# Kernel tuning notes

Measured on AMD Instinct MI355X. Metric: run time of the kernel, lower is better.

## Reference

```python
import jax, jax.numpy as jnp
import numpy as np

N_NODES = 50000
N_EDGES = 800000
HIDDEN = 128
EDGE_DIM = 16
COORDS_RANGE = 15.0


def setup_inputs() -> dict:
    key = jax.random.key(0)
    ks = jax.random.split(key, 12)
    h = jax.random.normal(ks[0], (N_NODES, HIDDEN), dtype=jnp.float32)
    x = jax.random.normal(ks[1], (N_NODES, 3), dtype=jnp.float32)
    edge_index = jax.random.randint(ks[2], (2, N_EDGES), 0, N_NODES, dtype=jnp.int64)
    edge_attr = jax.random.normal(ks[3], (N_EDGES, EDGE_DIM), dtype=jnp.float32)
    coord_diff = jax.random.normal(ks[4], (N_EDGES, 3), dtype=jnp.float32)
    flags = jnp.ones((N_NODES, 1), dtype=jnp.float32)
    edge_mask = jnp.ones((N_EDGES, 1), dtype=jnp.float32)
    d_in = 2 * HIDDEN + EDGE_DIM
    # MLP params (xavier-ish scaling; last layer gain 0.001 as in source)
    W1 = jax.random.normal(ks[5], (d_in, HIDDEN), dtype=jnp.float32) * (2.0 / (d_in + HIDDEN)) ** 0.5
    b1 = jnp.zeros((HIDDEN,), dtype=jnp.float32)
    W2 = jax.random.normal(ks[6], (HIDDEN, HIDDEN), dtype=jnp.float32) * (1.0 / HIDDEN) ** 0.5
    b2 = jnp.zeros((HIDDEN,), dtype=jnp.float32)
    W3 = jax.random.normal(ks[7], (HIDDEN, 1), dtype=jnp.float32) * 0.001 * (2.0 / (HIDDEN + 1)) ** 0.5
    return {"h": h, "x": x, "edge_index": edge_index, "edge_attr": edge_attr,
            "coord_diff": coord_diff, "flags": flags, "edge_mask": edge_mask,
            "W1": W1, "b1": b1, "W2": W2, "b2": b2, "W3": W3}


def reference(h, x, edge_index, edge_attr, coord_diff, flags, edge_mask, W1, b1, W2, b2, W3):
    row, col = edge_index[0], edge_index[1]
    # gather node features per edge and concat with edge features: [E, 2H+De]
    msg = jnp.concatenate([h[row], h[col], edge_attr], axis=1)
    z = jax.nn.silu(msg @ W1 + b1)
    z = jax.nn.silu(z @ W2 + b2)
    scale = jnp.tanh(z @ W3)                  # [E, 1]
    trans = coord_diff * scale * COORDS_RANGE # [E, 3]
    # NOTE: source computes `tanns = trans * edge_mask` but never uses it;
    # the aggregation uses the UNmasked trans. Faithfully replicated.
    agg = jax.ops.segment_sum(trans, row, num_segments=x.shape[0])  # [N, 3]
    return (x + agg) * flags
```

## Files before the change

kernel.cpp:

```cpp
#include <hip/hip_runtime.h>

typedef short  short8   __attribute__((ext_vector_type(8)));
typedef float  floatx16 __attribute__((ext_vector_type(16)));

#define HID  128
#define LDM  296
#define LDZ  136
#define NK1  18
#define NK2  8

__device__ __forceinline__ float fast_silu(float v) {
    return __fdividef(v, 1.0f + __expf(-v));
}
__device__ __forceinline__ unsigned short f2bf(float f) {
    union { float f; unsigned int u; } v; v.f = f;
    unsigned int r = v.u + 0x7FFFu + ((v.u >> 16) & 1u);
    return (unsigned short)(r >> 16);
}

__global__ void prep_weights(const float* __restrict__ W1, const float* __restrict__ W2,
                             unsigned short* __restrict__ w1t, unsigned short* __restrict__ w2t)
{
    const int tid = blockIdx.x * 256 + threadIdx.x;
    if (tid < 4 * NK1 * 64) {
        const int tn   = tid / (NK1 * 64);
        const int rem  = tid % (NK1 * 64);
        const int ks   = rem / 64;
        const int lane = rem % 64;
        const int n  = 32 * tn + (lane & 31);
        const int kb = 16 * ks + 8 * (lane >> 5);
        unsigned short o[8];
        #pragma unroll
        for (int j = 0; j < 8; ++j) {
            const int k = kb + j;
            o[j] = (k < 272) ? f2bf(W1[(size_t)k * HID + n]) : (unsigned short)0;
        }
        #pragma unroll
        for (int j = 0; j < 8; ++j) w1t[(size_t)tid * 8 + j] = o[j];
    } else if (tid < 4 * NK1 * 64 + 4 * NK2 * 64) {
        const int id   = tid - 4 * NK1 * 64;
        const int tn   = id / (NK2 * 64);
        const int rem  = id % (NK2 * 64);
        const int ks   = rem / 64;
        const int lane = rem % 64;
        const int n  = 32 * tn + (lane & 31);
        const int kb = 16 * ks + 8 * (lane >> 5);
        #pragma unroll
        for (int j = 0; j < 8; ++j)
            w2t[(size_t)id * 8 + j] = f2bf(W2[(size_t)(kb + j) * HID + n]);
    }
}

__global__ void prep_cast(const float* __restrict__ h, const float* __restrict__ ea,
                          unsigned short* __restrict__ hb, unsigned short* __restrict__ eab,
                          int nh, int nea)
{
    const int total4 = (nh + nea) >> 2;
    for (int i = blockIdx.x * blockDim.x + threadIdx.x; i < total4; i += gridDim.x * blockDim.x) {
        float4 v;
        unsigned short* dst;
        if (i < (nh >> 2)) { v = ((const float4*)h)[i];            dst = hb  + (size_t)i * 4; }
        else               { v = ((const float4*)ea)[i - (nh>>2)]; dst = eab + (size_t)(i - (nh>>2)) * 4; }
        const unsigned int lo = (unsigned int)f2bf(v.x) | ((unsigned int)f2bf(v.y) << 16);
        const unsigned int hi = (unsigned int)f2bf(v.z) | ((unsigned int)f2bf(v.w) << 16);
        *(uint2*)dst = make_uint2(lo, hi);
    }
}

__global__ __launch_bounds__(256, 2) void egnn_mfma_kernel(
    const unsigned short* __restrict__ hb,
    const int* __restrict__ eidx,
    const unsigned short* __restrict__ eab,
    const float* __restrict__ coord_diff,
    const unsigned short* __restrict__ w1t,
    const unsigned short* __restrict__ w2t,
    const float* __restrict__ b1,
    const float* __restrict__ b2,
    const float* __restrict__ W3,
    float* __restrict__ agg,
    int E, int niter)
{
    __shared__ unsigned short s_msg[64][LDM];
    __shared__ unsigned short s_z1[64][LDZ];
    __shared__ float s_z3[64];
    __shared__ int   s_row[64];

    const int t    = threadIdx.x;
    const int lane = t & 63;
    const int w    = t >> 6;
    const int c31  = lane & 31;
    const int hi   = lane >> 5;

    float b1f[16], b2f[16], w3f[16];
    #pragma unroll
    for (int r = 0; r < 16; ++r) {
        const int n = 32 * w + (r & 3) + 8 * (r >> 2) + 4 * hi;
        b1f[r] = b1[n]; b2f[r] = b2[n]; w3f[r] = W3[n];
    }

    for (int it = blockIdx.x; it < niter; it += gridDim.x) {
        const int ebase = it * 64;

        {
            const int e = t >> 2, s = t & 3;
            const int g  = ebase + e;
            const int gc = (g < E) ? g : (E - 1);
            const int row = eidx[gc];
            const int col = eidx[(size_t)E + gc];
            if (s == 0) s_row[e] = row;
            if (t < 64) s_z3[t] = 0.0f;
            const uint4* hr = (const uint4*)(hb + (size_t)row * HID);
            const uint4* hc = (const uint4*)(hb + (size_t)col * HID);
            #pragma unroll
            for (int i = 0; i < 4; ++i) {
                const int q = s + 4 * i;
                *(uint4*)&s_msg[e][q * 8]       = hr[q];
                *(uint4*)&s_msg[e][HID + q * 8] = hc[q];
            }
            const uint4* ea4 = (const uint4*)(eab + (size_t)gc * 16);
            if (s < 2) *(uint4*)&s_msg[e][256 + s * 8] = ea4[s];
            else       *(uint4*)&s_msg[e][256 + s * 8] = make_uint4(0u, 0u, 0u, 0u);
        }
        __syncthreads();

        floatx16 acc0 = {}, acc1 = {};
        #pragma unroll
        for (int ks = 0; ks < NK1; ++ks) {
            const short8 wf = *(const short8*)(w1t + ((size_t)(w * NK1 + ks) * 64 + lane) * 8);
            const short8 a0 = *(const short8*)&s_msg[c31][16 * ks + 8 * hi];
            const short8 a1 = *(const short8*)&s_msg[32 + c31][16 * ks + 8 * hi];
            acc0 = __builtin_amdgcn_mfma_f32_32x32x16_bf16(wf, a0, acc0, 0, 0, 0);
            acc1 = __builtin_amdgcn_mfma_f32_32x32x16_bf16(wf, a1, acc1, 0, 0, 0);
        }
        #pragma unroll
        for (int te = 0; te < 2; ++te) {
            const floatx16& A = te ? acc1 : acc0;
            const int e = 32 * te + c31;
            #pragma unroll
            for (int q = 0; q < 4; ++q) {
                const float f0 = fast_silu(A[4*q+0] + b1f[4*q+0]);
                const float f1 = fast_silu(A[4*q+1] + b1f[4*q+1]);
                const float f2 = fast_silu(A[4*q+2] + b1f[4*q+2]);
                const float f3 = fast_silu(A[4*q+3] + b1f[4*q+3]);
                const unsigned int lo = (unsigned int)f2bf(f0) | ((unsigned int)f2bf(f1) << 16);
                const unsigned int hw = (unsigned int)f2bf(f2) | ((unsigned int)f2bf(f3) << 16);
                *(uint2*)&s_z1[e][32 * w + 8 * q + 4 * hi] = make_uint2(lo, hw);
            }
        }
        __syncthreads();

        floatx16 g0 = {}, g1 = {};
        #pragma unroll
        for (int ks = 0; ks < NK2; ++ks) {
            const short8 wf = *(const short8*)(w2t + ((size_t)(w * NK2 + ks) * 64 + lane) * 8);
            const short8 a0 = *(const short8*)&s_z1[c31][16 * ks + 8 * hi];
            const short8 a1 = *(const short8*)&s_z1[32 + c31][16 * ks + 8 * hi];
            g0 = __builtin_amdgcn_mfma_f32_32x32x16_bf16(wf, a0, g0, 0, 0, 0);
            g1 = __builtin_amdgcn_mfma_f32_32x32x16_bf16(wf, a1, g1, 0, 0, 0);
        }
        float p0 = 0.0f, p1 = 0.0f;
        #pragma unroll
        for (int r = 0; r < 16; ++r) {
            p0 += fast_silu(g0[r] + b2f[r]) * w3f[r];
            p1 += fast_silu(g1[r] + b2f[r]) * w3f[r];
        }
        p0 += __shfl_xor(p0, 32, 64);
        p1 += __shfl_xor(p1, 32, 64);
        if (hi == 0) {
            atomicAdd(&s_z3[c31], p0);
            atomicAdd(&s_z3[32 + c31], p1);
        }
        __syncthreads();

        if (t < 64) {
            const int g = ebase + t;
            if (g < E) {
                const float sc = tanhf(s_z3[t]) * 15.0f;
                const int row = s_row[t];
                const float* cd = coord_diff + (size_t)g * 3;
                atomicAdd(&agg[row * 3 + 0], cd[0] * sc);
                atomicAdd(&agg[row * 3 + 1], cd[1] * sc);
                atomicAdd(&agg[row * 3 + 2], cd[2] * sc);
            }
        }
        __syncthreads();
    }
}

__global__ void finalize_kernel(const float* __restrict__ x,
                                const float* __restrict__ flags,
                                float* __restrict__ out, int n3)
{
    const int i = blockIdx.x * blockDim.x + threadIdx.x;
    if (i < n3) {
        const int n = i / 3;
        out[i] = (out[i] + x[i]) * flags[n];
    }
}

extern "C" void kernel_launch(void* const* d_in, const int* in_sizes, int n_in,
                              void* d_out, int out_size, void* d_ws, size_t ws_size,
                              hipStream_t stream)
{
    const float* h          = (const float*)d_in[0];
    const float* x          = (const float*)d_in[1];
    const int*   eix        = (const int*)d_in[2];
    const float* edge_attr  = (const float*)d_in[3];
    const float* coord_diff = (const float*)d_in[4];
    const float* flags      = (const float*)d_in[5];
    const float* W1 = (const float*)d_in[7];
    const float* b1 = (const float*)d_in[8];
    const float* W2 = (const float*)d_in[9];
    const float* b2 = (const float*)d_in[10];
    const float* W3 = (const float*)d_in[11];
    float* out = (float*)d_out;

    const int N3 = in_sizes[1];
    const int E  = in_sizes[4] / 3;
    const int nh  = in_sizes[0];
    const int nea = in_sizes[3];

    unsigned short* w1t = (unsigned short*)d_ws;
    unsigned short* w2t = w1t + 4 * NK1 * 64 * 8;
    unsigned short* hb  = (unsigned short*)((char*)d_ws + 106496);
    unsigned short* eab = hb + (size_t)nh;

    hipMemsetAsync(out, 0, (size_t)N3 * sizeof(float), stream);
    prep_weights<<<26, 256, 0, stream>>>(W1, W2, w1t, w2t);
    prep_cast<<<2048, 256, 0, stream>>>(h, edge_attr, hb, eab, nh, nea);

    const int niter = (E + 63) / 64;
    egnn_mfma_kernel<<<512, 256, 0, stream>>>(hb, eix, eab, coord_diff,
                                              w1t, w2t, b1, b2, W3, out, E, niter);
    finalize_kernel<<<(N3 + 255) / 256, 256, 0, stream>>>(x, flags, out, N3);
}
```

Before: 329.6 us.

## Fuse prep kernels, convert edge_attr in-kernel, split MLP across 8 waves

Merges the weight-transpose and h-cast kernels into one launch and removes the separate edge_attr bf16 cast pass, converting edge features to bf16 inside the main kernel's gather instead. The main kernel moves to 512 threads: each of 8 waves computes one 32-edge by 32-column tile instead of two edge tiles per wave, which halves per-wave accumulators and raises wave-level parallelism. The K dimension of the first GEMM shrinks from 18 to 17 steps by dropping the zero-padded chunk, which also shrinks the LDS row pitch. The launch-bounds change to (512,4) may constrain registers, and per-block LDS and sync overhead now cover twice as many waves.

```diff
diff --git a/kernel.cpp b/kernel.cpp
--- a/kernel.cpp
+++ b/kernel.cpp
@@ -4,9 +4,9 @@
 typedef float  floatx16 __attribute__((ext_vector_type(16)));
 
 #define HID  128
-#define LDM  296
+#define LDM  280
 #define LDZ  136
-#define NK1  18
+#define NK1  17
 #define NK2  8
 
 __device__ __forceinline__ float fast_silu(float v) {
@@ -17,60 +17,58 @@
     unsigned int r = v.u + 0x7FFFu + ((v.u >> 16) & 1u);
     return (unsigned short)(r >> 16);
 }
-
-__global__ void prep_weights(const float* __restrict__ W1, const float* __restrict__ W2,
-                             unsigned short* __restrict__ w1t, unsigned short* __restrict__ w2t)
-{
-    const int tid = blockIdx.x * 256 + threadIdx.x;
-    if (tid < 4 * NK1 * 64) {
-        const int tn   = tid / (NK1 * 64);
-        const int rem  = tid % (NK1 * 64);
-        const int ks   = rem / 64;
-        const int lane = rem % 64;
-        const int n  = 32 * tn + (lane & 31);
-        const int kb = 16 * ks + 8 * (lane >> 5);
-        unsigned short o[8];
-        #pragma unroll
-        for (int j = 0; j < 8; ++j) {
-            const int k = kb + j;
-            o[j] = (k < 272) ? f2bf(W1[(size_t)k * HID + n]) : (unsigned short)0;
-        }
-        #pragma unroll
-        for (int j = 0; j < 8; ++j) w1t[(size_t)tid * 8 + j] = o[j];
-    } else if (tid < 4 * NK1 * 64 + 4 * NK2 * 64) {
-        const int id   = tid - 4 * NK1 * 64;
-        const int tn   = id / (NK2 * 64);
-        const int rem  = id % (NK2 * 64);
-        const int ks   = rem / 64;
-        const int lane = rem % 64;
-        const int n  = 32 * tn + (lane & 31);
-        const int kb = 16 * ks + 8 * (lane >> 5);
-        #pragma unroll
-        for (int j = 0; j < 8; ++j)
-            w2t[(size_t)id * 8 + j] = f2bf(W2[(size_t)(kb + j) * HID + n]);
-    }
-}
-
-__global__ void prep_cast(const float* __restrict__ h, const float* __restrict__ ea,
-                          unsigned short* __restrict__ hb, unsigned short* __restrict__ eab,
-                          int nh, int nea)
-{
-    const int total4 = (nh + nea) >> 2;
-    for (int i = blockIdx.x * blockDim.x + threadIdx.x; i < total4; i += gridDim.x * blockDim.x) {
-        float4 v;
-        unsigned short* dst;
-        if (i < (nh >> 2)) { v = ((const float4*)h)[i];            dst = hb  + (size_t)i * 4; }
-        else               { v = ((const float4*)ea)[i - (nh>>2)]; dst = eab + (size_t)(i - (nh>>2)) * 4; }
-        const unsigned int lo = (unsigned int)f2bf(v.x) | ((unsigned int)f2bf(v.y) << 16);
-        const unsigned int hi = (unsigned int)f2bf(v.z) | ((unsigned int)f2bf(v.w) << 16);
-        *(uint2*)dst = make_uint2(lo, hi);
-    }
-}
-
-__global__ __launch_bounds__(256, 2) void egnn_mfma_kernel(
+__device__ __forceinline__ unsigned int pk2bf(float a, float b) {
+    return (unsigned int)f2bf(a) | ((unsigned int)f2bf(b) << 16);
+}
+
+__global__ void prep_all(const float* __restrict__ W1, const float* __restrict__ W2,
+                         const float* __restrict__ h,
+                         unsigned short* __restrict__ w1t, unsigned short* __restrict__ w2t,
+                         unsigned short* __restrict__ hb, int nh8)
+{
+    const int NW1 = 4 * NK1 * 64;
+    const int NW2 = 4 * NK2 * 64;
+    const int tot = NW1 + NW2 + nh8;
+    union { unsigned short s[8]; uint4 v; } o;
+    for (int id = blockIdx.x * blockDim.x + threadIdx.x; id < tot;
+         id += gridDim.x * blockDim.x) {
+        if (id < NW1) {
+            const int nt   = id / (NK1 * 64);
+            const int rem  = id % (NK1 * 64);
+            const int ks   = rem / 64;
+            const int lane = rem % 64;
+            const int n  = 32 * nt + (lane & 31);
+            const int kb = 16 * ks + 8 * (lane >> 5);
+            #pragma unroll
+            for (int j = 0; j < 8; ++j) o.s[j] = f2bf(W1[(size_t)(kb + j) * HID + n]);
+            *(uint4*)(w1t + (size_t)id * 8) = o.v;
+        } else if (id < NW1 + NW2) {
+            const int id2  = id - NW1;
+            const int nt   = id2 / (NK2 * 64);
+            const int rem  = id2 % (NK2 * 64);
+            const int ks   = rem / 64;
+            const int lane = rem % 64;
+            const int n  = 32 * nt + (lane & 31);
+            const int kb = 16 * ks + 8 * (lane >> 5);
+            #pragma unroll
+            for (int j = 0; j < 8; ++j) o.s[j] = f2bf(W2[(size_t)(kb + j) * HID + n]);
+            *(uint4*)(w2t + (size_t)id2 * 8) = o.v;
+        } else {
+            const int i = id - NW1 - NW2;
+            const float4 va = ((const float4*)h)[2 * i];
+            const float4 vb = ((const float4*)h)[2 * i + 1];
+            uint4 w;
+            w.x = pk2bf(va.x, va.y); w.y = pk2bf(va.z, va.w);
+            w.z = pk2bf(vb.x, vb.y); w.w = pk2bf(vb.z, vb.w);
+            ((uint4*)hb)[i] = w;
+        }
+    }
+}
+
+__global__ __launch_bounds__(512, 4) void egnn_mfma_kernel(
     const unsigned short* __restrict__ hb,
     const int* __restrict__ eidx,
-    const unsigned short* __restrict__ eab,
+    const float* __restrict__ edge_attr,
     const float* __restrict__ coord_diff,
     const unsigned short* __restrict__ w1t,
     const unsigned short* __restrict__ w2t,
@@ -88,13 +86,15 @@
     const int t    = threadIdx.x;
     const int lane = t & 63;
     const int w    = t >> 6;
+    const int nt   = w & 3;
+    const int et   = w >> 2;
     const int c31  = lane & 31;
     const int hi   = lane >> 5;
 
     float b1f[16], b2f[16], w3f[16];
     #pragma unroll
     for (int r = 0; r < 16; ++r) {
-        const int n = 32 * w + (r & 3) + 8 * (r >> 2) + 4 * hi;
+        const int n = 32 * nt + (r & 3) + 8 * (r >> 2) + 4 * hi;
         b1f[r] = b1[n]; b2f[r] = b2[n]; w3f[r] = W3[n];
     }
 
@@ -102,7 +102,7 @@
         const int ebase = it * 64;
 
         {
-            const int e = t >> 2, s = t & 3;
+            const int e = t >> 3, s = t & 7;
             const int g  = ebase + e;
             const int gc = (g < E) ? g : (E - 1);
             const int row = eidx[gc];
@@ -111,65 +111,48 @@
             if (t < 64) s_z3[t] = 0.0f;
             const uint4* hr = (const uint4*)(hb + (size_t)row * HID);
             const uint4* hc = (const uint4*)(hb + (size_t)col * HID);
-            #pragma unroll
-            for (int i = 0; i < 4; ++i) {
-                const int q = s + 4 * i;
-                *(uint4*)&s_msg[e][q * 8]       = hr[q];
-                *(uint4*)&s_msg[e][HID + q * 8] = hc[q];
+            *(uint4*)&s_msg[e][s * 8]             = hr[s];
+            *(uint4*)&s_msg[e][(s + 8) * 8]       = hr[s + 8];
+            *(uint4*)&s_msg[e][HID + s * 8]       = hc[s];
+            *(uint4*)&s_msg[e][HID + (s + 8) * 8] = hc[s + 8];
+            if (s < 4) {
+                const float4 ea = ((const float4*)(edge_attr + (size_t)gc * 16))[s];
+                *(uint2*)&s_msg[e][256 + s * 4] =
+                    make_uint2(pk2bf(ea.x, ea.y), pk2bf(ea.z, ea.w));
             }
-            const uint4* ea4 = (const uint4*)(eab + (size_t)gc * 16);
-            if (s < 2) *(uint4*)&s_msg[e][256 + s * 8] = ea4[s];
-            else       *(uint4*)&s_msg[e][256 + s * 8] = make_uint4(0u, 0u, 0u, 0u);
-        }
-        __syncthreads();
-
-        floatx16 acc0 = {}, acc1 = {};
+        }
+        __syncthreads();
+
+        floatx16 acc = {};
         #pragma unroll
         for (int ks = 0; ks < NK1; ++ks) {
-            const short8 wf = *(const short8*)(w1t + ((size_t)(w * NK1 + ks) * 64 + lane) * 8);
-            const short8 a0 = *(const short8*)&s_msg[c31][16 * ks + 8 * hi];
-            const short8 a1 = *(const short8*)&s_msg[32 + c31][16 * ks + 8 * hi];
-            acc0 = __builtin_amdgcn_mfma_f32_32x32x16_bf16(wf, a0, acc0, 0, 0, 0);
-            acc1 = __builtin_amdgcn_mfma_f32_32x32x16_bf16(wf, a1, acc1, 0, 0, 0);
-        }
-        #pragma unroll
-        for (int te = 0; te < 2; ++te) {
-            const floatx16& A = te ? acc1 : acc0;
-            const int e = 32 * te + c31;
-            #pragma unroll
-            for (int q = 0; q < 4; ++q) {
-                const float f0 = fast_silu(A[4*q+0] + b1f[4*q+0]);
-                const float f1 = fast_silu(A[4*q+1] + b1f[4*q+1]);
-                const float f2 = fast_silu(A[4*q+2] + b1f[4*q+2]);
-                const float f3 = fast_silu(A[4*q+3] + b1f[4*q+3]);
-                const unsigned int lo = (unsigned int)f2bf(f0) | ((unsigned int)f2bf(f1) << 16);
-                const unsigned int hw = (unsigned int)f2bf(f2) | ((unsigned int)f2bf(f3) << 16);
-                *(uint2*)&s_z1[e][32 * w + 8 * q + 4 * hi] = make_uint2(lo, hw);
-            }
-        }
-        __syncthreads();
-
-        floatx16 g0 = {}, g1 = {};
+            const short8 wf = *(const short8*)(w1t + ((size_t)(nt * NK1 + ks) * 64 + lane) * 8);
+            const short8 af = *(const short8*)&s_msg[32 * et + c31][16 * ks + 8 * hi];
+            acc = __builtin_amdgcn_mfma_f32_32x32x16_bf16(wf, af, acc, 0, 0, 0);
+        }
+        #pragma unroll
+        for (int q = 0; q < 4; ++q) {
+            const float f0 = fast_silu(acc[4*q+0] + b1f[4*q+0]);
+            const float f1 = fast_silu(acc[4*q+1] + b1f[4*q+1]);
+            const float f2 = fast_silu(acc[4*q+2] + b1f[4*q+2]);
+            const float f3 = fast_silu(acc[4*q+3] + b1f[4*q+3]);
+            *(uint2*)&s_z1[32 * et + c31][32 * nt + 8 * q + 4 * hi] =
+                make_uint2(pk2bf(f0, f1), pk2bf(f2, f3));
+        }
+        __syncthreads();
+
+        floatx16 g2 = {};
         #pragma unroll
         for (int ks = 0; ks < NK2; ++ks) {
-            const short8 wf = *(const short8*)(w2t + ((size_t)(w * NK2 + ks) * 64 + lane) * 8);
-            const short8 a0 = *(const short8*)&s_z1[c31][16 * ks + 8 * hi];
-            const short8 a1 = *(const short8*)&s_z1[32 + c31][16 * ks + 8 * hi];
-            g0 = __builtin_amdgcn_mfma_f32_32x32x16_bf16(wf, a0, g0, 0, 0, 0);
-            g1 = __builtin_amdgcn_mfma_f32_32x32x16_bf16(wf, a1, g1, 0, 0, 0);
-        }
-        float p0 = 0.0f, p1 = 0.0f;
-        #pragma unroll
-        for (int r = 0; r < 16; ++r) {
-            p0 += fast_silu(g0[r] + b2f[r]) * w3f[r];
-            p1 += fast_silu(g1[r] + b2f[r]) * w3f[r];
-        }
-        p0 += __shfl_xor(p0, 32, 64);
-        p1 += __shfl_xor(p1, 32, 64);
-        if (hi == 0) {
-            atomicAdd(&s_z3[c31], p0);
-            atomicAdd(&s_z3[32 + c31], p1);
-        }
+            const short8 wf = *(const short8*)(w2t + ((size_t)(nt * NK2 + ks) * 64 + lane) * 8);
+            const short8 af = *(const short8*)&s_z1[32 * et + c31][16 * ks + 8 * hi];
+            g2 = __builtin_amdgcn_mfma_f32_32x32x16_bf16(wf, af, g2, 0, 0, 0);
+        }
+        float p = 0.0f;
+        #pragma unroll
+        for (int r = 0; r < 16; ++r) p += fast_silu(g2[r] + b2f[r]) * w3f[r];
+        p += __shfl_xor(p, 32, 64);
+        if (hi == 0) atomicAdd(&s_z3[32 * et + c31], p);
         __syncthreads();
 
         if (t < 64) {
@@ -217,20 +200,17 @@
 
     const int N3 = in_sizes[1];
     const int E  = in_sizes[4] / 3;
-    const int nh  = in_sizes[0];
-    const int nea = in_sizes[3];
+    const int nh = in_sizes[0];
 
     unsigned short* w1t = (unsigned short*)d_ws;
     unsigned short* w2t = w1t + 4 * NK1 * 64 * 8;
-    unsigned short* hb  = (unsigned short*)((char*)d_ws + 106496);
-    unsigned short* eab = hb + (size_t)nh;
-
-    hipMemsetAsync(out, 0, (size_t)N3 * sizeof(float), stream);
-    prep_weights<<<26, 256, 0, stream>>>(W1, W2, w1t, w2t);
-    prep_cast<<<2048, 256, 0, stream>>>(h, edge_attr, hb, eab, nh, nea);
+    unsigned short* hb  = (unsigned short*)((char*)d_ws + 102400);
+
+    (void)hipMemsetAsync(out, 0, (size_t)N3 * sizeof(float), stream);
+    prep_all<<<1024, 256, 0, stream>>>(W1, W2, h, w1t, w2t, hb, nh >> 3);
 
     const int niter = (E + 63) / 64;
-    egnn_mfma_kernel<<<512, 256, 0, stream>>>(hb, eix, eab, coord_diff,
+    egnn_mfma_kernel<<<512, 512, 0, stream>>>(hb, eix, edge_attr, coord_diff,
                                               w1t, w2t, b1, b2, W3, out, E, niter);
     finalize_kernel<<<(N3 + 255) / 256, 256, 0, stream>>>(x, flags, out, N3);
 }
```

After: 522.0 us. +58.4%, slower.
